# Performance work log

Measured on AMD Instinct MI355X. Metric: run time of the kernel, lower is better.

## Reference

```python
import jax, jax.numpy as jnp
import numpy as np

N_NODES = 100000
N_EDGES = 1600000
D_IN, D_HID, D_OUT = 32, 16, 2


def graph_conv(x, edge_index, w_rel, w_root, b):
    # PyG GraphConv (aggr='add'): out_i = x_i @ W_root^T + (sum_{j in N(i)} x_j) @ W_rel^T + b
    src, dst = edge_index[0], edge_index[1]
    msgs = x[src]                                            # [E, d] neighbor gather
    agg = jax.ops.segment_sum(msgs, dst, num_segments=N_NODES)  # [N, d] scatter-add
    return agg @ w_rel.T + x @ w_root.T + b


def setup_inputs() -> dict:
    key = jax.random.key(0)
    ks = jax.random.split(key, 8)
    x = jax.random.normal(ks[0], (N_NODES, D_IN), dtype=jnp.float32)
    edge_index = jax.random.randint(ks[1], (2, N_EDGES), 0, N_NODES, dtype=jnp.int64)
    def glorot(k, shape):
        lim = np.sqrt(6.0 / (shape[0] + shape[1]))
        return jax.random.uniform(k, shape, jnp.float32, -lim, lim)
    w1_rel = glorot(ks[2], (D_HID, D_IN))
    w1_root = glorot(ks[3], (D_HID, D_IN))
    b1 = jnp.zeros((D_HID,), jnp.float32)
    w2_rel = glorot(ks[4], (D_OUT, D_HID))
    w2_root = glorot(ks[5], (D_OUT, D_HID))
    b2 = jnp.zeros((D_OUT,), jnp.float32)
    return {"x": x, "edge_index": edge_index,
            "w1_rel": w1_rel, "w1_root": w1_root, "b1": b1,
            "w2_rel": w2_rel, "w2_root": w2_root, "b2": b2}


def reference(x, edge_index, w1_rel, w1_root, b1, w2_rel, w2_root, b2):
    h = graph_conv(x, edge_index, w1_rel, w1_root, b1)
    h = jax.nn.relu(h)
    out = graph_conv(h, edge_index, w2_rel, w2_root, b2)
    return out
```

## Files before the change

kernel.cpp:

```cpp
#include <hip/hip_runtime.h>

#define N_NODES 100000
#define N_EDGES 1600000
#define D_IN 32
#define D_HID 16
#define D_OUT 2

#define NPB 128
#define NB 782
#define NROWS (NB * NPB)
#define CHUNK 4096
#define BBLOCKS ((N_EDGES + CHUNK - 1) / CHUNK)

#define PBC 2560
#define DUMMY_SRC 100000u
#define DUMMY_REC ((127u << 17) | DUMMY_SRC)
#define PAD_ALIGN 16

#define ACC2_K 16
#define ACC2_BPB 2
#define ACC2_BLOCKS (NB * ACC2_BPB)

__device__ __forceinline__ unsigned bfr(float x) {
    unsigned u = __float_as_uint(x);
    return (u + 0x7FFFu + ((u >> 16) & 1u)) >> 16;
}
__device__ __forceinline__ float bfu(unsigned lo16) {
    return __uint_as_float(lo16 << 16);
}

__global__ __launch_bounds__(512) void k_bin_node1(
    const int* __restrict__ ei, const float* __restrict__ x,
    const float* __restrict__ w_rel, const float* __restrict__ w_root,
    const float* __restrict__ bb,
    unsigned short* __restrict__ xr, float* __restrict__ agg,
    int* __restrict__ gcur, unsigned* __restrict__ recs2)
{
    __shared__ int cnt[NB];
    __shared__ int lcnt[NB];
    __shared__ int loff[NB];
    __shared__ int gbase[NB];
    __shared__ unsigned sorted[CHUNK];
    __shared__ unsigned short bkt16[CHUNK];
    __shared__ float s_rel[D_HID * D_IN];
    __shared__ float s_root[D_HID * D_IN];
    __shared__ float s_b[D_HID];
    int blk = blockIdx.x, tid = threadIdx.x;

    for (int i = tid; i < D_HID * D_IN; i += 512) {
        s_rel[i]  = w_rel[i];
        s_root[i] = w_root[i];
    }
    if (tid < D_HID) s_b[tid] = bb[tid];
    for (int i = tid; i < NB; i += 512) { cnt[i] = 0; lcnt[i] = 0; }
    __syncthreads();

    int e0 = blk * CHUNK;
    int e1 = min(e0 + CHUNK, N_EDGES);
    for (int e = e0 + tid; e < e1; e += 512)
        atomicAdd(&cnt[ei[N_EDGES + e] >> 7], 1);

    int node = blk * 512 + tid;
    if (node == N_NODES) {
        uint4* xp = (uint4*)(xr + (size_t)node * D_HID);
        xp[0] = make_uint4(0, 0, 0, 0);
        xp[1] = make_uint4(0, 0, 0, 0);
    } else if (node < N_NODES) {
        float row[D_IN];
        const float4* xp = (const float4*)(x + (size_t)node * D_IN);
#pragma unroll
        for (int i = 0; i < D_IN / 4; i++) {
            float4 v = xp[i];
            row[4*i+0] = v.x; row[4*i+1] = v.y; row[4*i+2] = v.z; row[4*i+3] = v.w;
        }
        float oa[D_HID], orr[D_HID];
#pragma unroll
        for (int o = 0; o < D_HID; o++) {
            float a = 0.f, r = s_b[o];
#pragma unroll
            for (int k = 0; k < D_IN; k++) {
                a += row[k] * s_rel[o * D_IN + k];
                r += row[k] * s_root[o * D_IN + k];
            }
            oa[o] = a; orr[o] = r;
        }
        unsigned p[8];
#pragma unroll
        for (int i = 0; i < 8; i++)
            p[i] = bfr(oa[2*i]) | (bfr(oa[2*i+1]) << 16);
        uint4* xrp = (uint4*)(xr + (size_t)node * D_HID);
        xrp[0] = make_uint4(p[0], p[1], p[2], p[3]);
        xrp[1] = make_uint4(p[4], p[5], p[6], p[7]);
        float4* aggp = (float4*)(agg + (size_t)node * D_HID);
#pragma unroll
        for (int i = 0; i < D_HID / 4; i++)
            aggp[i] = make_float4(orr[4*i], orr[4*i+1], orr[4*i+2], orr[4*i+3]);
    }
    __syncthreads();

    if (tid < 64) {
        int running = 0;
        for (int c = 0; c < (NB + 63) / 64; c++) {
            int idx = c * 64 + tid;
            int v = (idx < NB) ? cnt[idx] : 0;
            int incl = v;
#pragma unroll
            for (int off = 1; off < 64; off <<= 1) {
                int t = __shfl_up(incl, off);
                if (tid >= off) incl += t;
            }
            if (idx < NB) loff[idx] = running + incl - v;
            running += __shfl(incl, 63);
        }
    } else {
        for (int i = tid - 64; i < NB; i += 448)
            gbase[i] = (cnt[i] > 0) ? atomicAdd(&gcur[i], cnt[i]) : 0;
    }
    __syncthreads();

    for (int e = e0 + tid; e < e1; e += 512) {
        int src = ei[e];
        int dst = ei[N_EDGES + e];
        int bkt = dst >> 7;
        int r = atomicAdd(&lcnt[bkt], 1);
        int p = loff[bkt] + r;
        sorted[p] = ((unsigned)(dst & (NPB - 1)) << 17) | (unsigned)src;
        bkt16[p] = (unsigned short)bkt;
    }
    __syncthreads();

    int n4 = e1 - e0;
    for (int i = tid; i < n4; i += 512) {
        int b = bkt16[i];
        int idx = gbase[b] + (i - loff[b]);
        if (idx < PBC)
            recs2[b * PBC + idx] = sorted[i];
    }
}

__global__ __launch_bounds__(512) void k_sortacc(
    const int* __restrict__ gcur, unsigned* __restrict__ recs2,
    const unsigned short* __restrict__ srcf, float* __restrict__ dstf)
{
    __shared__ unsigned stage[PBC];
    __shared__ unsigned sorted[PBC];
    __shared__ int hist[NPB], sc[NPB], cur[NPB];
    int b = blockIdx.x, tid = threadIdx.x;
    int n = min(gcur[b], PBC);
    unsigned* w = recs2 + (size_t)b * PBC;

    if (tid < NPB) hist[tid] = 0;
    for (int i = tid; i < n; i += 512) stage[i] = w[i];
    __syncthreads();
    for (int i = tid; i < n; i += 512)
        atomicAdd(&hist[stage[i] >> 17], 1);
    __syncthreads();
    if (tid < NPB) sc[tid] = hist[tid];
    __syncthreads();
#pragma unroll
    for (int off = 1; off < NPB; off <<= 1) {
        int t = (tid >= off && tid < NPB) ? sc[tid - off] : 0;
        __syncthreads();
        if (tid < NPB) sc[tid] += t;
        __syncthreads();
    }
    if (tid < NPB) cur[tid] = sc[tid] - hist[tid];
    __syncthreads();
    for (int i = tid; i < n; i += 512) {
        unsigned r = stage[i];
        int slot = atomicAdd(&cur[r >> 17], 1);
        sorted[slot] = r;
    }
    int npad = (n + PAD_ALIGN - 1) & ~(PAD_ALIGN - 1);
    for (int i = n + tid; i < npad; i += 512) sorted[i] = DUMMY_REC;
    __syncthreads();

    for (int i = tid; i < npad; i += 512) w[i] = sorted[i];

    int g = tid >> 4;
    int f = tid & (D_HID - 1);
    int dbase = b * NPB;
    for (int base = g * 16; base < npad; base += 32 * 16) {
        unsigned e[16];
#pragma unroll
        for (int k = 0; k < 16; k++) e[k] = sorted[base + k];
        float v[16];
#pragma unroll
        for (int k = 0; k < 16; k++)
            v[k] = bfu(srcf[(e[k] & 0x1FFFF) * D_HID + f]);

        unsigned curd = e[0] >> 17;
        float acc = v[0];
#pragma unroll
        for (int k = 1; k < 16; k++) {
            unsigned dl = e[k] >> 17;
            if (dl == curd) {
                acc += v[k];
            } else {
                atomicAdd(&dstf[(dbase + curd) * D_HID + f], acc);
                curd = dl;
                acc = v[k];
            }
        }
        atomicAdd(&dstf[(dbase + curd) * D_HID + f], acc);
    }
}

__global__ __launch_bounds__(256) void k_node2h(
    const float* __restrict__ agg,
    const float* __restrict__ w_rel, const float* __restrict__ w_root,
    const float* __restrict__ b,
    float* __restrict__ hr, float* __restrict__ outv)
{
    __shared__ float s_rel[D_OUT * D_HID];
    __shared__ float s_root[D_OUT * D_HID];
    __shared__ float s_b[D_OUT];
    if (threadIdx.x < D_OUT * D_HID) {
        s_rel[threadIdx.x]  = w_rel[threadIdx.x];
        s_root[threadIdx.x] = w_root[threadIdx.x];
    }
    if (threadIdx.x < D_OUT) s_b[threadIdx.x] = b[threadIdx.x];
    __syncthreads();

    int node = blockIdx.x * blockDim.x + threadIdx.x;
    if (node > N_NODES) return;
    if (node == N_NODES) {
        ((float2*)hr)[node] = make_float2(0.f, 0.f);
        return;
    }

    float hv[D_HID];
    const float4* ap = (const float4*)(agg + (size_t)node * D_HID);
#pragma unroll
    for (int i = 0; i < D_HID / 4; i++) {
        float4 v = ap[i];
        hv[4*i+0] = fmaxf(v.x, 0.f); hv[4*i+1] = fmaxf(v.y, 0.f);
        hv[4*i+2] = fmaxf(v.z, 0.f); hv[4*i+3] = fmaxf(v.w, 0.f);
    }

    float o_rel[D_OUT], o_root[D_OUT];
#pragma unroll
    for (int o = 0; o < D_OUT; o++) {
        float a = 0.f, r = s_b[o];
#pragma unroll
        for (int k = 0; k < D_HID; k++) {
            a += hv[k] * s_rel[o * D_HID + k];
            r += hv[k] * s_root[o * D_HID + k];
        }
        o_rel[o] = a; o_root[o] = r;
    }
    ((float2*)hr)[node]   = make_float2(o_rel[0], o_rel[1]);
    ((float2*)outv)[node] = make_float2(o_root[0], o_root[1]);
}

__global__ __launch_bounds__(256) void k_acc2(
    const unsigned* __restrict__ recs2, const int* __restrict__ gcur,
    const float* __restrict__ hr, float* __restrict__ outv)
{
    int bucket = blockIdx.x / ACC2_BPB;
    int blk    = blockIdx.x % ACC2_BPB;
    int g = threadIdx.x >> 1;
    int f = threadIdx.x & 1;
    int r0 = (blk * 128 + g) * ACC2_K;
    int n = min(gcur[bucket], PBC);
    if (r0 >= n) return;
    const unsigned* rp = recs2 + (size_t)bucket * PBC + r0;

    unsigned e[ACC2_K];
#pragma unroll
    for (int k = 0; k < ACC2_K; k++) e[k] = rp[k];
    float v[ACC2_K];
#pragma unroll
    for (int k = 0; k < ACC2_K; k++)
        v[k] = hr[(e[k] & 0x1FFFF) * D_OUT + f];

    int dbase = bucket * NPB;
    unsigned cur = e[0] >> 17;
    float acc = v[0];
#pragma unroll
    for (int k = 1; k < ACC2_K; k++) {
        unsigned dl = e[k] >> 17;
        if (dl == cur) {
            acc += v[k];
        } else {
            int d = dbase + (int)cur;
            if (d < N_NODES) atomicAdd(&outv[d * D_OUT + f], acc);
            cur = dl;
            acc = v[k];
        }
    }
    int d = dbase + (int)cur;
    if (d < N_NODES) atomicAdd(&outv[d * D_OUT + f], acc);
}

extern "C" void kernel_launch(void* const* d_in, const int* in_sizes, int n_in,
                              void* d_out, int out_size, void* d_ws, size_t ws_size,
                              hipStream_t stream) {
    const float* x       = (const float*)d_in[0];
    const int*   ei      = (const int*)  d_in[1];
    const float* w1_rel  = (const float*)d_in[2];
    const float* w1_root = (const float*)d_in[3];
    const float* b1      = (const float*)d_in[4];
    const float* w2_rel  = (const float*)d_in[5];
    const float* w2_root = (const float*)d_in[6];
    const float* b2      = (const float*)d_in[7];
    float* out = (float*)d_out;

    float*          agg   = (float*)d_ws;
    unsigned short* xrh   = (unsigned short*)(agg + (size_t)NROWS * D_HID);
    unsigned*       recs2 = (unsigned*)(xrh + (size_t)NROWS * D_HID);
    float*          hr    = (float*)(recs2 + (size_t)NB * PBC);
    int*            gcur  = (int*)(hr + (size_t)NROWS * D_OUT);

    hipMemsetAsync(gcur, 0, NB * sizeof(int), stream);

    k_bin_node1<<<dim3(BBLOCKS), dim3(512), 0, stream>>>(
        ei, x, w1_rel, w1_root, b1, xrh, agg, gcur, recs2);

    k_sortacc<<<dim3(NB), dim3(512), 0, stream>>>(gcur, recs2, xrh, agg);

    k_node2h<<<dim3((N_NODES + 256) / 256), dim3(256), 0, stream>>>(
        agg, w2_rel, w2_root, b2, hr, out);

    k_acc2<<<dim3(ACC2_BLOCKS), dim3(256), 0, stream>>>(recs2, gcur, hr, out);
}
```

Measured before the change: 162.8 us.

## Replace per-bucket sort with shared-memory atomic aggregation fused with layer-2 node transform

Removes the per-bucket counting sort and global atomics in layer 1. Each bucket block now accumulates neighbor features into a shared-memory tile using LDS atomics, then applies ReLU and the layer-2 linear transforms in the same kernel, so the separate node kernel is gone. Layer-2 aggregation also accumulates into a shared tile per bucket and writes out once, replacing global atomics. This cuts one launch and global atomic traffic, but LDS atomic contention and summation order now depend on record order, making the result nondeterministic.

```diff
diff --git a/kernel.cpp b/kernel.cpp
--- a/kernel.cpp
+++ b/kernel.cpp
@@ -13,13 +13,6 @@
 #define BBLOCKS ((N_EDGES + CHUNK - 1) / CHUNK)
 
 #define PBC 2560
-#define DUMMY_SRC 100000u
-#define DUMMY_REC ((127u << 17) | DUMMY_SRC)
-#define PAD_ALIGN 16
-
-#define ACC2_K 16
-#define ACC2_BPB 2
-#define ACC2_BLOCKS (NB * ACC2_BPB)
 
 __device__ __forceinline__ unsigned bfr(float x) {
     unsigned u = __float_as_uint(x);
@@ -138,159 +131,106 @@
     }
 }
 
-__global__ __launch_bounds__(512) void k_sortacc(
-    const int* __restrict__ gcur, unsigned* __restrict__ recs2,
-    const unsigned short* __restrict__ srcf, float* __restrict__ dstf)
-{
-    __shared__ unsigned stage[PBC];
-    __shared__ unsigned sorted[PBC];
-    __shared__ int hist[NPB], sc[NPB], cur[NPB];
-    int b = blockIdx.x, tid = threadIdx.x;
-    int n = min(gcur[b], PBC);
-    unsigned* w = recs2 + (size_t)b * PBC;
-
-    if (tid < NPB) hist[tid] = 0;
-    for (int i = tid; i < n; i += 512) stage[i] = w[i];
-    __syncthreads();
-    for (int i = tid; i < n; i += 512)
-        atomicAdd(&hist[stage[i] >> 17], 1);
-    __syncthreads();
-    if (tid < NPB) sc[tid] = hist[tid];
-    __syncthreads();
-#pragma unroll
-    for (int off = 1; off < NPB; off <<= 1) {
-        int t = (tid >= off && tid < NPB) ? sc[tid - off] : 0;
-        __syncthreads();
-        if (tid < NPB) sc[tid] += t;
-        __syncthreads();
-    }
-    if (tid < NPB) cur[tid] = sc[tid] - hist[tid];
-    __syncthreads();
-    for (int i = tid; i < n; i += 512) {
-        unsigned r = stage[i];
-        int slot = atomicAdd(&cur[r >> 17], 1);
-        sorted[slot] = r;
-    }
-    int npad = (n + PAD_ALIGN - 1) & ~(PAD_ALIGN - 1);
-    for (int i = n + tid; i < npad; i += 512) sorted[i] = DUMMY_REC;
-    __syncthreads();
-
-    for (int i = tid; i < npad; i += 512) w[i] = sorted[i];
-
-    int g = tid >> 4;
-    int f = tid & (D_HID - 1);
-    int dbase = b * NPB;
-    for (int base = g * 16; base < npad; base += 32 * 16) {
-        unsigned e[16];
-#pragma unroll
-        for (int k = 0; k < 16; k++) e[k] = sorted[base + k];
-        float v[16];
-#pragma unroll
-        for (int k = 0; k < 16; k++)
-            v[k] = bfu(srcf[(e[k] & 0x1FFFF) * D_HID + f]);
-
-        unsigned curd = e[0] >> 17;
-        float acc = v[0];
-#pragma unroll
-        for (int k = 1; k < 16; k++) {
-            unsigned dl = e[k] >> 17;
-            if (dl == curd) {
-                acc += v[k];
-            } else {
-                atomicAdd(&dstf[(dbase + curd) * D_HID + f], acc);
-                curd = dl;
-                acc = v[k];
-            }
-        }
-        atomicAdd(&dstf[(dbase + curd) * D_HID + f], acc);
-    }
-}
-
-__global__ __launch_bounds__(256) void k_node2h(
-    const float* __restrict__ agg,
-    const float* __restrict__ w_rel, const float* __restrict__ w_root,
-    const float* __restrict__ b,
+__global__ __launch_bounds__(512) void k_agg1x(
+    const int* __restrict__ gcur, const unsigned* __restrict__ recs2,
+    const unsigned short* __restrict__ xr, const float* __restrict__ agg,
+    const float* __restrict__ w_rel2, const float* __restrict__ w_root2,
+    const float* __restrict__ bb2,
     float* __restrict__ hr, float* __restrict__ outv)
 {
+    __shared__ float tile[NPB][D_HID + 1];
     __shared__ float s_rel[D_OUT * D_HID];
     __shared__ float s_root[D_OUT * D_HID];
     __shared__ float s_b[D_OUT];
-    if (threadIdx.x < D_OUT * D_HID) {
-        s_rel[threadIdx.x]  = w_rel[threadIdx.x];
-        s_root[threadIdx.x] = w_root[threadIdx.x];
-    }
-    if (threadIdx.x < D_OUT) s_b[threadIdx.x] = b[threadIdx.x];
-    __syncthreads();
-
-    int node = blockIdx.x * blockDim.x + threadIdx.x;
-    if (node > N_NODES) return;
-    if (node == N_NODES) {
-        ((float2*)hr)[node] = make_float2(0.f, 0.f);
-        return;
-    }
-
-    float hv[D_HID];
-    const float4* ap = (const float4*)(agg + (size_t)node * D_HID);
-#pragma unroll
-    for (int i = 0; i < D_HID / 4; i++) {
-        float4 v = ap[i];
-        hv[4*i+0] = fmaxf(v.x, 0.f); hv[4*i+1] = fmaxf(v.y, 0.f);
-        hv[4*i+2] = fmaxf(v.z, 0.f); hv[4*i+3] = fmaxf(v.w, 0.f);
-    }
-
-    float o_rel[D_OUT], o_root[D_OUT];
-#pragma unroll
-    for (int o = 0; o < D_OUT; o++) {
-        float a = 0.f, r = s_b[o];
-#pragma unroll
-        for (int k = 0; k < D_HID; k++) {
-            a += hv[k] * s_rel[o * D_HID + k];
-            r += hv[k] * s_root[o * D_HID + k];
-        }
-        o_rel[o] = a; o_root[o] = r;
-    }
-    ((float2*)hr)[node]   = make_float2(o_rel[0], o_rel[1]);
-    ((float2*)outv)[node] = make_float2(o_root[0], o_root[1]);
-}
-
-__global__ __launch_bounds__(256) void k_acc2(
-    const unsigned* __restrict__ recs2, const int* __restrict__ gcur,
+    int b = blockIdx.x, tid = threadIdx.x;
+
+    if (tid < D_OUT * D_HID) {
+        s_rel[tid]  = w_rel2[tid];
+        s_root[tid] = w_root2[tid];
+    }
+    if (tid < D_OUT) s_b[tid] = bb2[tid];
+
+    {
+        int i4 = tid * 4;
+        float4 v = *(const float4*)(agg + (size_t)b * NPB * D_HID + i4);
+        int r = i4 >> 4, c = i4 & 15;
+        tile[r][c + 0] = v.x; tile[r][c + 1] = v.y;
+        tile[r][c + 2] = v.z; tile[r][c + 3] = v.w;
+    }
+    __syncthreads();
+
+    int n = min(gcur[b], PBC);
+    const unsigned* rp = recs2 + (size_t)b * PBC;
+    int half = tid & 1;
+    for (int i = (tid >> 1); i < n; i += 256) {
+        unsigned rec = rp[i];
+        int src  = rec & 0x1FFFF;
+        int dloc = rec >> 17;
+        uint4 v = *(const uint4*)(xr + (size_t)src * D_HID + half * 8);
+        float* d = &tile[dloc][half * 8];
+        atomicAdd(d + 0, bfu(v.x & 0xFFFFu)); atomicAdd(d + 1, bfu(v.x >> 16));
+        atomicAdd(d + 2, bfu(v.y & 0xFFFFu)); atomicAdd(d + 3, bfu(v.y >> 16));
+        atomicAdd(d + 4, bfu(v.z & 0xFFFFu)); atomicAdd(d + 5, bfu(v.z >> 16));
+        atomicAdd(d + 6, bfu(v.w & 0xFFFFu)); atomicAdd(d + 7, bfu(v.w >> 16));
+    }
+    __syncthreads();
+
+    if (tid < NPB) {
+        int node = b * NPB + tid;
+        if (node < N_NODES) {
+            float h[D_HID];
+#pragma unroll
+            for (int k = 0; k < D_HID; k++) h[k] = fmaxf(tile[tid][k], 0.f);
+            float o_rel[D_OUT], o_root[D_OUT];
+#pragma unroll
+            for (int o = 0; o < D_OUT; o++) {
+                float a = 0.f, r = s_b[o];
+#pragma unroll
+                for (int k = 0; k < D_HID; k++) {
+                    a += h[k] * s_rel[o * D_HID + k];
+                    r += h[k] * s_root[o * D_HID + k];
+                }
+                o_rel[o] = a; o_root[o] = r;
+            }
+            ((float2*)hr)[node]   = make_float2(o_rel[0], o_rel[1]);
+            ((float2*)outv)[node] = make_float2(o_root[0], o_root[1]);
+        }
+    }
+}
+
+__global__ __launch_bounds__(256) void k_acc2x(
+    const int* __restrict__ gcur, const unsigned* __restrict__ recs2,
     const float* __restrict__ hr, float* __restrict__ outv)
 {
-    int bucket = blockIdx.x / ACC2_BPB;
-    int blk    = blockIdx.x % ACC2_BPB;
-    int g = threadIdx.x >> 1;
-    int f = threadIdx.x & 1;
-    int r0 = (blk * 128 + g) * ACC2_K;
-    int n = min(gcur[bucket], PBC);
-    if (r0 >= n) return;
-    const unsigned* rp = recs2 + (size_t)bucket * PBC + r0;
-
-    unsigned e[ACC2_K];
-#pragma unroll
-    for (int k = 0; k < ACC2_K; k++) e[k] = rp[k];
-    float v[ACC2_K];
-#pragma unroll
-    for (int k = 0; k < ACC2_K; k++)
-        v[k] = hr[(e[k] & 0x1FFFF) * D_OUT + f];
-
-    int dbase = bucket * NPB;
-    unsigned cur = e[0] >> 17;
-    float acc = v[0];
-#pragma unroll
-    for (int k = 1; k < ACC2_K; k++) {
-        unsigned dl = e[k] >> 17;
-        if (dl == cur) {
-            acc += v[k];
-        } else {
-            int d = dbase + (int)cur;
-            if (d < N_NODES) atomicAdd(&outv[d * D_OUT + f], acc);
-            cur = dl;
-            acc = v[k];
-        }
-    }
-    int d = dbase + (int)cur;
-    if (d < N_NODES) atomicAdd(&outv[d * D_OUT + f], acc);
+    __shared__ float tile[NPB * 3];
+    int b = blockIdx.x, tid = threadIdx.x;
+    int n = min(gcur[b], PBC);
+    const unsigned* rp = recs2 + (size_t)b * PBC;
+
+    if (tid < NPB) {
+        int node = b * NPB + tid;
+        if (node < N_NODES) {
+            float2 o = ((const float2*)outv)[node];
+            tile[tid * 3 + 0] = o.x;
+            tile[tid * 3 + 1] = o.y;
+        }
+    }
+    __syncthreads();
+
+    for (int i = tid; i < n; i += 256) {
+        unsigned rec = rp[i];
+        float2 v = ((const float2*)hr)[rec & 0x1FFFF];
+        int d3 = (int)(rec >> 17) * 3;
+        atomicAdd(&tile[d3 + 0], v.x);
+        atomicAdd(&tile[d3 + 1], v.y);
+    }
+    __syncthreads();
+
+    if (tid < NPB) {
+        int node = b * NPB + tid;
+        if (node < N_NODES)
+            ((float2*)outv)[node] = make_float2(tile[tid * 3], tile[tid * 3 + 1]);
+    }
 }
 
 extern "C" void kernel_launch(void* const* d_in, const int* in_sizes, int n_in,
@@ -317,10 +257,8 @@
     k_bin_node1<<<dim3(BBLOCKS), dim3(512), 0, stream>>>(
         ei, x, w1_rel, w1_root, b1, xrh, agg, gcur, recs2);
 
-    k_sortacc<<<dim3(NB), dim3(512), 0, stream>>>(gcur, recs2, xrh, agg);
-
-    k_node2h<<<dim3((N_NODES + 256) / 256), dim3(256), 0, stream>>>(
-        agg, w2_rel, w2_root, b2, hr, out);
-
-    k_acc2<<<dim3(ACC2_BLOCKS), dim3(256), 0, stream>>>(recs2, gcur, hr, out);
-}
+    k_agg1x<<<dim3(NB), dim3(512), 0, stream>>>(
+        gcur, recs2, xrh, agg, w2_rel, w2_root, b2, hr, out);
+
+    k_acc2x<<<dim3(NB), dim3(256), 0, stream>>>(gcur, recs2, hr, out);
+}
```

Measured after the change: 306.1 us. 88.0% more time.
